# Optimization experiments

Measured on AMD Instinct MI355X. Metric: run time of the kernel, lower is better.

Reference implementation:

```python
import math
import jax, jax.numpy as jnp
import numpy as np

CNT_HEAD, D_IN, D_OUT, D_KEY, D_VALUE = 16, 1024, 1024, 64, 64
BATCH, SEQ = 4, 2048
IS_SCALED, IS_CAUSAL = True, True


def _xavier(key, shape, d1, d2):
    a = math.sqrt(6.0 / (d1 + d2))
    return jax.random.uniform(key, shape, jnp.float32, -a, a)


def setup_inputs() -> dict:
    key = jax.random.key(0)
    kx, kq, kk, kv, ko = jax.random.split(key, 5)
    x = jax.random.normal(kx, (BATCH, SEQ, D_IN), jnp.float32)
    mask = jnp.zeros((BATCH, SEQ), dtype=bool)  # padding mask, True = masked out
    W_q = _xavier(kq, (CNT_HEAD, D_IN, D_KEY), D_IN, CNT_HEAD * D_KEY)
    W_k = _xavier(kk, (CNT_HEAD, D_IN, D_KEY), D_IN, CNT_HEAD * D_KEY)
    W_v = _xavier(kv, (CNT_HEAD, D_IN, D_VALUE), D_IN, CNT_HEAD * D_VALUE)
    W_o = _xavier(ko, (CNT_HEAD, D_VALUE, D_OUT), CNT_HEAD * D_VALUE, D_OUT)
    return {"x": x, "mask": mask, "W_q": W_q, "W_k": W_k, "W_v": W_v, "W_o": W_o}


def reference(x, mask, W_q, W_k, W_v, W_o):
    seq_len = x.shape[-2]
    # per-head projections: (h, d_in, d) x (b, s, d_in) -> (b, h, s, d)
    Q = jnp.einsum('hjk,bsj->bhsk', W_q, x)
    K = jnp.einsum('hjk,bsj->bhsk', W_k, x)
    V = jnp.einsum('hjk,bsj->bhsk', W_v, x)
    # combined mask -> (b, 1, s, s), True = masked
    causal = jnp.triu(jnp.ones((seq_len, seq_len), dtype=bool), k=1)
    if IS_CAUSAL:
        m = mask[..., None, :] | causal  # (b, s, s)
    else:
        m = jnp.broadcast_to(mask[..., None, :], (mask.shape[0], seq_len, seq_len))
    m = m[..., None, :, :]  # (b, 1, s, s)
    scores = jnp.einsum('bhik,bhjk->bhij', Q, K)
    scores = jnp.where(m, -jnp.inf, scores)
    if IS_SCALED:
        scores = scores / math.sqrt(D_KEY)
    weights = jax.nn.softmax(scores, axis=-1)
    values = jnp.einsum('bhij,bhjd->bhid', weights, V)
    return jnp.einsum('hjk,bhlj->blk', W_o, values)
```

## Files before the change

### kernel.cpp

```cpp
#include <hip/hip_runtime.h>
#include <hip/hip_bf16.h>

typedef __attribute__((ext_vector_type(4))) float f32x4;
typedef __attribute__((ext_vector_type(8))) short s16x8;
typedef __attribute__((ext_vector_type(8))) unsigned short u16x8;
typedef __attribute__((ext_vector_type(4))) unsigned short u16x4;

#define BATCH 4
#define SEQ   2048
#define DIN   1024
#define NHEAD 16
#define HD3   3072
#define DOUT  1024

__device__ __forceinline__ unsigned short f2bf(float f) {
  __hip_bfloat16 h = __float2bfloat16(f);
  return __builtin_bit_cast(unsigned short, h);
}

__device__ __forceinline__ float fmax3(float a, float b, float c) {
  return fmaxf(fmaxf(a, b), c);
}

#if __has_builtin(__builtin_amdgcn_exp2f)
__device__ __forceinline__ float fast_exp2(float x) { return __builtin_amdgcn_exp2f(x); }
#else
__device__ __forceinline__ float fast_exp2(float x) { return exp2f(x); }
#endif

typedef const __attribute__((address_space(1))) unsigned int* gas_t;
typedef __attribute__((address_space(3))) unsigned int* las_t;
__device__ __forceinline__ void gload16(const void* g, void* l) {
  __builtin_amdgcn_global_load_lds((gas_t)g, (las_t)l, 16, 0, 0);
}

__global__ __launch_bounds__(256) void k_cvt_x(const float* __restrict__ x,
                                               unsigned short* __restrict__ xb, int n4) {
  int i = blockIdx.x * 256 + threadIdx.x;
  int stride = gridDim.x * 256;
  for (; i < n4; i += stride) {
    float4 v = reinterpret_cast<const float4*>(x)[i];
    ushort4 o;
    o.x = f2bf(v.x); o.y = f2bf(v.y); o.z = f2bf(v.z); o.w = f2bf(v.w);
    reinterpret_cast<ushort4*>(xb)[i] = o;
  }
}

__global__ __launch_bounds__(256) void k_cvt_w(const float* __restrict__ W,
                                               unsigned short* __restrict__ dst) {
  __shared__ float t[64][65];
  int h = blockIdx.x, j0 = blockIdx.y * 64;
  int c = threadIdx.x & 63, r0 = threadIdx.x >> 6;
#pragma unroll
  for (int r = r0; r < 64; r += 4)
    t[r][c] = W[h * 65536 + (j0 + r) * 64 + c];
  __syncthreads();
#pragma unroll
  for (int k = r0; k < 64; k += 4)
    dst[(size_t)(h * 64 + k) * 1024 + j0 + c] = f2bf(t[c][k]);
}

__global__ __launch_bounds__(256) void k_cvt_wo(const float* __restrict__ W,
                                                unsigned short* __restrict__ dst) {
  __shared__ float t[64][65];
  int h = blockIdx.x, n0 = blockIdx.y * 64;
  int c = threadIdx.x & 63, r0 = threadIdx.x >> 6;
#pragma unroll
  for (int d = r0; d < 64; d += 4)
    t[d][c] = W[h * 65536 + d * 1024 + n0 + c];
  __syncthreads();
#pragma unroll
  for (int n = r0; n < 64; n += 4)
    dst[(size_t)(n0 + n) * 1024 + h * 64 + c] = f2bf(t[c][n]);
}

__global__ __launch_bounds__(256) void k_transpose_v(const unsigned short* __restrict__ QKV,
                                                     unsigned short* __restrict__ Vt) {
  __shared__ unsigned short t[64 * 80];
  int tid = threadIdx.x;
  int s0 = blockIdx.x * 64;
  int h = blockIdx.y, b = blockIdx.z;
  const unsigned short* src = QKV + (size_t)b * SEQ * HD3 + 2048 + (size_t)h * 64;
#pragma unroll
  for (int c = 0; c < 2; ++c) {
    int slot = tid + c * 256;
    int s = slot >> 3, g = slot & 7;
    u16x8 v = *reinterpret_cast<const u16x8*>(src + (size_t)(s0 + s) * HD3 + g * 8);
    *reinterpret_cast<u16x8*>(&t[s * 80 + (g ^ (s >> 3)) * 8]) = v;
  }
  __syncthreads();
  unsigned short* dst = Vt + (size_t)(b * NHEAD + h) * 64 * SEQ + s0;
#pragma unroll
  for (int c = 0; c < 2; ++c) {
    int slot = tid + c * 256;
    int d = slot >> 3, c8 = slot & 7;
    u16x8 v;
#pragma unroll
    for (int j = 0; j < 8; ++j) {
      int s = ((c8 >> 2) << 5) + ((j >> 2) << 4) + ((c8 & 3) << 2) + (j & 3);
      v[j] = t[s * 80 + (((d >> 3) ^ (s >> 3)) * 8) + (d & 7)];
    }
    *reinterpret_cast<u16x8*>(dst + (size_t)d * SEQ + c8 * 8) = v;
  }
}

__device__ __forceinline__ void stout(float* p, float v) { *p = v; }
__device__ __forceinline__ void stout(unsigned short* p, float v) { *p = f2bf(v); }

template <typename OutT>
__global__ __launch_bounds__(256) void gemm_bt(const unsigned short* __restrict__ A,
                                               const unsigned short* __restrict__ Bt,
                                               OutT* __restrict__ C, int M, int N, int K) {
  __shared__ unsigned short As[3][128 * 32];
  __shared__ unsigned short Bs[3][128 * 32];
  int tid = threadIdx.x, w = tid >> 6, lane = tid & 63;
  int lr = lane & 15, lk = lane >> 4;
  int m0 = blockIdx.x * 128, n0 = blockIdx.y * 128;
  int wm = (w >> 1) * 64, wn = (w & 1) * 64;
  const f32x4 z = {0.f, 0.f, 0.f, 0.f};
  f32x4 acc[4][4];
#pragma unroll
  for (int m = 0; m < 4; ++m)
#pragma unroll
    for (int n = 0; n < 4; ++n) acc[m][n] = z;

  int r0 = w * 32 + (lane >> 2);
  int r1 = r0 + 16;
  int scol = (((lane & 3) ^ ((lane >> 2) & 3)) * 8);
  const unsigned short* pA0 = A + (size_t)(m0 + r0) * K + scol;
  const unsigned short* pA1 = A + (size_t)(m0 + r1) * K + scol;
  const unsigned short* pB0 = Bt + (size_t)(n0 + r0) * K + scol;
  const unsigned short* pB1 = Bt + (size_t)(n0 + r1) * K + scol;

#define GSTAGE(bi_, ko_)                                              \
  {                                                                   \
    gload16(pA0 + (ko_), (char*)As[bi_] + (w * 2 + 0) * 1024);        \
    gload16(pB0 + (ko_), (char*)Bs[bi_] + (w * 2 + 0) * 1024);        \
    gload16(pA1 + (ko_), (char*)As[bi_] + (w * 2 + 1) * 1024);        \
    gload16(pB1 + (ko_), (char*)Bs[bi_] + (w * 2 + 1) * 1024);        \
  }

  GSTAGE(0, 0)
  GSTAGE(1, 32)
  asm volatile("s_waitcnt vmcnt(4)" ::: "memory");
  __builtin_amdgcn_s_barrier();
  asm volatile("" ::: "memory");

  const int T = K >> 5;
  int bi = 0;
  int cka = lk ^ (lr & 3);
  for (int t = 0; t < T; ++t) {
    if (t + 2 < T) {
      int bs = bi + 2; if (bs >= 3) bs -= 3;
      GSTAGE(bs, (t + 2) * 32)
    }
    s16x8 af[4], bfr[4];
#pragma unroll
    for (int m = 0; m < 4; ++m)
      af[m] = *reinterpret_cast<const s16x8*>(&As[bi][(wm + m * 16 + lr) * 32 + cka * 8]);
#pragma unroll
    for (int n = 0; n < 4; ++n)
      bfr[n] = *reinterpret_cast<const s16x8*>(&Bs[bi][(wn + n * 16 + lr) * 32 + cka * 8]);
#pragma unroll
    for (int m = 0; m < 4; ++m)
#pragma unroll
      for (int n = 0; n < 4; ++n)
        acc[m][n] = __builtin_amdgcn_mfma_f32_16x16x32_bf16(af[m], bfr[n], acc[m][n], 0, 0, 0);
    asm volatile("s_waitcnt lgkmcnt(0)" ::: "memory");
    if (t + 2 < T)
      asm volatile("s_waitcnt vmcnt(4)" ::: "memory");
    else
      asm volatile("s_waitcnt vmcnt(0)" ::: "memory");
    __builtin_amdgcn_s_barrier();
    asm volatile("" ::: "memory");
    if (++bi >= 3) bi = 0;
  }
#undef GSTAGE

#pragma unroll
  for (int m = 0; m < 4; ++m)
#pragma unroll
    for (int n = 0; n < 4; ++n)
#pragma unroll
      for (int r = 0; r < 4; ++r) {
        int row = m0 + wm + m * 16 + lk * 4 + r;
        int col = n0 + wn + n * 16 + lr;
        stout(&C[(size_t)row * N + col], acc[m][n][r]);
      }
}

__global__ __launch_bounds__(256) void attn_kernel(const unsigned short* __restrict__ QKV,
                                                   const unsigned short* __restrict__ Vt,
                                                   unsigned short* __restrict__ Oa) {
  __shared__ unsigned short Ks[2][2][64 * 64];
  __shared__ unsigned short Vs[2][2][64 * 64];
  int tid = threadIdx.x, w = tid >> 6, lane = tid & 63;
  int lr = lane & 15, lk = lane >> 4;
  int bx = blockIdx.x;
  int bh = bx & 63;
  int qbi = 15 - (bx >> 6);
  int h = bh & 15, b = bh >> 4;
  int q0 = qbi * 128 + w * 32;
  const unsigned short* base = QKV + (size_t)b * SEQ * HD3;
  const unsigned short* vtb = Vt + (size_t)(b * NHEAD + h) * 64 * SEQ;
  const float cl = 0.1803368801111204f;
  const f32x4 z = {0.f, 0.f, 0.f, 0.f};

  s16x8 qf[2][2];
#pragma unroll
  for (int mf = 0; mf < 2; ++mf)
#pragma unroll
    for (int kfi = 0; kfi < 2; ++kfi)
      qf[mf][kfi] = *reinterpret_cast<const s16x8*>(
          base + (size_t)(q0 + mf * 16 + lr) * HD3 + h * 64 + kfi * 32 + lk * 8);

  f32x4 o[4][2], lacc[2];
#pragma unroll
  for (int nfd = 0; nfd < 4; ++nfd)
#pragma unroll
    for (int mf = 0; mf < 2; ++mf) o[nfd][mf] = z;
  lacc[0] = z; lacc[1] = z;
  float m_[2] = {-1e30f, -1e30f};
  s16x8 ones;
#pragma unroll
  for (int e = 0; e < 8; ++e) ones[e] = (short)0x3F80;

  const int nt = qbi + 1;

  int xr = (lr & 7) << 4;
  int off8[4][2];
#pragma unroll
  for (int nf = 0; nf < 4; ++nf)
#pragma unroll
    for (int kfi = 0; kfi < 2; ++kfi)
      off8[nf][kfi] = (nf * 16 + lr) * 128 + ((kfi * 64 + lk * 16) ^ xr);

  int srow0 = w * 16 + (lane >> 3);
  int cbs = ((lane & 7) * 16) ^ ((srow0 & 7) << 4);
  const char* pk0 = (const char*)(base + 1024 + h * 64 + (size_t)srow0 * HD3) + cbs;
  const char* pk1 = pk0 + (size_t)8 * HD3 * 2;
  const char* pv0 = (const char*)(vtb + (size_t)srow0 * SEQ) + cbs;
  const char* pv1 = pv0 + (size_t)8 * SEQ * 2;
  const size_t KSUB = (size_t)64 * HD3 * 2;
  const size_t KADV = (size_t)128 * HD3 * 2;
  const size_t VADV = 256;

#define STAGE(BS)                                                       \
  {                                                                     \
    gload16(pk0, (char*)&Ks[(BS)][0][0] + (w * 2 + 0) * 1024);          \
    gload16(pk0 + KSUB, (char*)&Ks[(BS)][1][0] + (w * 2 + 0) * 1024);   \
    gload16(pv0, (char*)&Vs[(BS)][0][0] + (w * 2 + 0) * 1024);          \
    gload16(pv0 + 128, (char*)&Vs[(BS)][1][0] + (w * 2 + 0) * 1024);    \
    gload16(pk1, (char*)&Ks[(BS)][0][0] + (w * 2 + 1) * 1024);          \
    gload16(pk1 + KSUB, (char*)&Ks[(BS)][1][0] + (w * 2 + 1) * 1024);   \
    gload16(pv1, (char*)&Vs[(BS)][0][0] + (w * 2 + 1) * 1024);          \
    gload16(pv1 + 128, (char*)&Vs[(BS)][1][0] + (w * 2 + 1) * 1024);    \
    pk0 += KADV; pk1 += KADV; pv0 += VADV; pv1 += VADV;                 \
  }

#define SUBTILE(BI, S, KB)                                                                \
  if ((KB) <= q0 + 31) {                                                                  \
    s16x8 kfr[4][2];                                                                      \
    _Pragma("unroll") for (int nf = 0; nf < 4; ++nf)                                      \
    _Pragma("unroll") for (int kfi = 0; kfi < 2; ++kfi)                                   \
      kfr[nf][kfi] = *reinterpret_cast<const s16x8*>(                                     \
          (const char*)&Ks[(BI)][(S)][0] + off8[nf][kfi]);                                \
    f32x4 st[4][2];                                                                       \
    _Pragma("unroll") for (int nf = 0; nf < 4; ++nf)                                      \
    _Pragma("unroll") for (int mf = 0; mf < 2; ++mf)                                      \
      st[nf][mf] = __builtin_amdgcn_mfma_f32_16x16x32_bf16(kfr[nf][0], qf[mf][0], z, 0, 0, 0); \
    _Pragma("unroll") for (int nf = 0; nf < 4; ++nf)                                      \
    _Pragma("unroll") for (int mf = 0; mf < 2; ++mf)                                      \
      st[nf][mf] = __builtin_amdgcn_mfma_f32_16x16x32_bf16(kfr[nf][1], qf[mf][1],         \
                                                           st[nf][mf], 0, 0, 0);          \
    if ((KB) + 63 > q0) {                                                                 \
      _Pragma("unroll") for (int nf = 0; nf < 4; ++nf)                                    \
      _Pragma("unroll") for (int mf = 0; mf < 2; ++mf)                                    \
      _Pragma("unroll") for (int r = 0; r < 4; ++r)                                       \
        if ((KB) + nf * 16 + lk * 4 + r > q0 + mf * 16 + lr) st[nf][mf][r] = -1e30f;      \
    }                                                                                     \
    s16x8 pf[2][2];                                                                       \
    _Pragma("unroll") for (int mf = 0; mf < 2; ++mf) {                                    \
      float t0 = fmax3(st[0][mf][0], st[0][mf][1], st[0][mf][2]);                         \
      float t1 = fmax3(st[0][mf][3], st[1][mf][0], st[1][mf][1]);                         \
      float t2 = fmax3(st[1][mf][2], st[1][mf][3], st[2][mf][0]);                         \
      float t3 = fmax3(st[2][mf][1], st[2][mf][2], st[2][mf][3]);                         \
      float t4 = fmax3(st[3][mf][0], st[3][mf][1], st[3][mf][2]);                         \
      float pm = fmaxf(fmax3(t0, t1, t2), fmax3(t3, t4, st[3][mf][3]));                   \
      pm = fmaxf(pm, __shfl_xor(pm, 16));                                                 \
      pm = fmaxf(pm, __shfl_xor(pm, 32));                                                 \
      pm *= cl;                                                                           \
      if (!__all(pm <= m_[mf] + 8.0f)) {                                                  \
        float mnew = fmaxf(m_[mf], pm);                                                   \
        float sc = fast_exp2(m_[mf] - mnew);                                              \
        m_[mf] = mnew;                                                                    \
        _Pragma("unroll") for (int nfd = 0; nfd < 4; ++nfd)                               \
        _Pragma("unroll") for (int r = 0; r < 4; ++r) o[nfd][mf][r] *= sc;                \
        _Pragma("unroll") for (int r = 0; r < 4; ++r) lacc[mf][r] *= sc;                  \
      }                                                                                   \
      float p[4][4];                                                                      \
      _Pragma("unroll") for (int nf = 0; nf < 4; ++nf)                                    \
      _Pragma("unroll") for (int r = 0; r < 4; ++r)                                       \
        p[nf][r] = fast_exp2(fmaf(st[nf][mf][r], cl, -m_[mf]));                           \
      union { s16x8 v; unsigned short e[8]; } pu0, pu1;                                   \
      _Pragma("unroll") for (int j2 = 0; j2 < 4; ++j2) {                                  \
        pu0.e[j2] = f2bf(p[0][j2]);                                                       \
        pu0.e[4 + j2] = f2bf(p[1][j2]);                                                   \
        pu1.e[j2] = f2bf(p[2][j2]);                                                       \
        pu1.e[4 + j2] = f2bf(p[3][j2]);                                                   \
      }                                                                                   \
      pf[mf][0] = pu0.v;                                                                  \
      pf[mf][1] = pu1.v;                                                                  \
    }                                                                                     \
    _Pragma("unroll") for (int mf = 0; mf < 2; ++mf)                                      \
    _Pragma("unroll") for (int ks = 0; ks < 2; ++ks)                                      \
      lacc[mf] = __builtin_amdgcn_mfma_f32_16x16x32_bf16(ones, pf[mf][ks],                \
                                                         lacc[mf], 0, 0, 0);              \
    _Pragma("unroll") for (int nfd = 0; nfd < 4; ++nfd)                                   \
    _Pragma("unroll") for (int ks = 0; ks < 2; ++ks) {                                    \
      s16x8 vf = *reinterpret_cast<const s16x8*>(                                         \
          (const char*)&Vs[(BI)][(S)][0] + off8[nfd][ks]);                                \
      _Pragma("unroll") for (int mf = 0; mf < 2; ++mf)                                    \
        o[nfd][mf] = __builtin_amdgcn_mfma_f32_16x16x32_bf16(vf, pf[mf][ks],              \
                                                             o[nfd][mf], 0, 0, 0);        \
    }                                                                                     \
  }

#define TILE(BI)                                                                          \
  {                                                                                       \
    if (kt + 1 < nt) STAGE((BI) ^ 1)                                                      \
    int kb = kt * 128;                                                                    \
    SUBTILE(BI, 0, kb)                                                                    \
    SUBTILE(BI, 1, kb + 64)                                                               \
    asm volatile("s_waitcnt lgkmcnt(0)" ::: "memory");                                    \
    asm volatile("s_waitcnt vmcnt(0)" ::: "memory");                                      \
    __builtin_amdgcn_s_barrier();                                                         \
    asm volatile("" ::: "memory");                                                        \
    ++kt;                                                                                 \
  }

  STAGE(0)
  asm volatile("s_waitcnt vmcnt(0)" ::: "memory");
  __builtin_amdgcn_s_barrier();
  asm volatile("" ::: "memory");

  int kt = 0;
  for (;;) {
    TILE(0)
    if (kt == nt) break;
    TILE(1)
    if (kt == nt) break;
  }
#undef TILE
#undef SUBTILE
#undef STAGE

#pragma unroll
  for (int mf = 0; mf < 2; ++mf) {
    float inv = 1.0f / lacc[mf][0];
    size_t rowoff = (size_t)(b * SEQ + q0 + mf * 16 + lr) * 1024 + h * 64;
#pragma unroll
    for (int nfd = 0; nfd < 4; ++nfd) {
      u16x4 ov;
#pragma unroll
      for (int r = 0; r < 4; ++r) ov[r] = f2bf(o[nfd][mf][r] * inv);
      *reinterpret_cast<u16x4*>(Oa + rowoff + nfd * 16 + lk * 4) = ov;
    }
  }
}

extern "C" void kernel_launch(void* const* d_in, const int* in_sizes, int n_in,
                              void* d_out, int out_size, void* d_ws, size_t ws_size,
                              hipStream_t stream) {
  const float* x  = (const float*)d_in[0];
  const float* Wq = (const float*)d_in[2];
  const float* Wk = (const float*)d_in[3];
  const float* Wv = (const float*)d_in[4];
  const float* Wo = (const float*)d_in[5];
  float* out = (float*)d_out;

  char* ws = (char*)d_ws;
  unsigned short* xb   = (unsigned short*)(ws);
  unsigned short* Wqkv = (unsigned short*)(ws + 16777216);
  unsigned short* Wot  = (unsigned short*)(ws + 23068672);
  unsigned short* QKV  = (unsigned short*)(ws + 25165824);
  unsigned short* Oa   = (unsigned short*)(ws + 75497472);
  unsigned short* Vtp  = xb;

  k_cvt_x<<<2048, 256, 0, stream>>>(x, xb, (BATCH * SEQ * DIN) / 4);
  dim3 wg(16, 16);
  k_cvt_w<<<wg, 256, 0, stream>>>(Wq, Wqkv);
  k_cvt_w<<<wg, 256, 0, stream>>>(Wk, Wqkv + 1024 * 1024);
  k_cvt_w<<<wg, 256, 0, stream>>>(Wv, Wqkv + 2 * 1024 * 1024);
  k_cvt_wo<<<wg, 256, 0, stream>>>(Wo, Wot);

  gemm_bt<unsigned short><<<dim3(64, 24), 256, 0, stream>>>(xb, Wqkv, QKV, 8192, 3072, 1024);
  k_transpose_v<<<dim3(32, NHEAD, BATCH), 256, 0, stream>>>(QKV, Vtp);
  attn_kernel<<<dim3(1024), 256, 0, stream>>>(QKV, Vtp, Oa);
  gemm_bt<float><<<dim3(64, 8), 256, 0, stream>>>(Oa, Wot, out, 8192, 1024, 1024);
}
```

Before: 199.8 us.

## Fuse V transpose into QKV GEMM epilogue and merge weight conversions

The QKV projection GEMM now writes the V columns directly in transposed per-head layout to a separate buffer, and stores only Q and K with row stride 2048. This removes the standalone V transpose kernel and its extra read and write of V. The four weight-conversion launches are also merged into one kernel indexed by blockIdx.z, cutting launch overhead. In exchange, the V epilogue does strided 8-byte stores across sequence rows, which may coalesce less well than the old row-major stores.

```diff
diff --git a/kernel.cpp b/kernel.cpp
--- a/kernel.cpp
+++ b/kernel.cpp
@@ -10,7 +10,7 @@
 #define SEQ   2048
 #define DIN   1024
 #define NHEAD 16
-#define HD3   3072
+#define QKW   2048
 #define DOUT  1024
 
 __device__ __forceinline__ unsigned short f2bf(float f) {
@@ -46,61 +46,34 @@
   }
 }
 
-__global__ __launch_bounds__(256) void k_cvt_w(const float* __restrict__ W,
-                                               unsigned short* __restrict__ dst) {
+__global__ __launch_bounds__(256) void k_cvt_wall(const float* __restrict__ Wq,
+                                                  const float* __restrict__ Wk,
+                                                  const float* __restrict__ Wv,
+                                                  const float* __restrict__ Wo,
+                                                  unsigned short* __restrict__ Wqkv,
+                                                  unsigned short* __restrict__ Wot) {
   __shared__ float t[64][65];
-  int h = blockIdx.x, j0 = blockIdx.y * 64;
+  int zi = blockIdx.z;
   int c = threadIdx.x & 63, r0 = threadIdx.x >> 6;
-#pragma unroll
-  for (int r = r0; r < 64; r += 4)
-    t[r][c] = W[h * 65536 + (j0 + r) * 64 + c];
-  __syncthreads();
-#pragma unroll
-  for (int k = r0; k < 64; k += 4)
-    dst[(size_t)(h * 64 + k) * 1024 + j0 + c] = f2bf(t[c][k]);
-}
-
-__global__ __launch_bounds__(256) void k_cvt_wo(const float* __restrict__ W,
-                                                unsigned short* __restrict__ dst) {
-  __shared__ float t[64][65];
-  int h = blockIdx.x, n0 = blockIdx.y * 64;
-  int c = threadIdx.x & 63, r0 = threadIdx.x >> 6;
-#pragma unroll
-  for (int d = r0; d < 64; d += 4)
-    t[d][c] = W[h * 65536 + d * 1024 + n0 + c];
-  __syncthreads();
-#pragma unroll
-  for (int n = r0; n < 64; n += 4)
-    dst[(size_t)(n0 + n) * 1024 + h * 64 + c] = f2bf(t[c][n]);
-}
-
-__global__ __launch_bounds__(256) void k_transpose_v(const unsigned short* __restrict__ QKV,
-                                                     unsigned short* __restrict__ Vt) {
-  __shared__ unsigned short t[64 * 80];
-  int tid = threadIdx.x;
-  int s0 = blockIdx.x * 64;
-  int h = blockIdx.y, b = blockIdx.z;
-  const unsigned short* src = QKV + (size_t)b * SEQ * HD3 + 2048 + (size_t)h * 64;
-#pragma unroll
-  for (int c = 0; c < 2; ++c) {
-    int slot = tid + c * 256;
-    int s = slot >> 3, g = slot & 7;
-    u16x8 v = *reinterpret_cast<const u16x8*>(src + (size_t)(s0 + s) * HD3 + g * 8);
-    *reinterpret_cast<u16x8*>(&t[s * 80 + (g ^ (s >> 3)) * 8]) = v;
-  }
-  __syncthreads();
-  unsigned short* dst = Vt + (size_t)(b * NHEAD + h) * 64 * SEQ + s0;
-#pragma unroll
-  for (int c = 0; c < 2; ++c) {
-    int slot = tid + c * 256;
-    int d = slot >> 3, c8 = slot & 7;
-    u16x8 v;
-#pragma unroll
-    for (int j = 0; j < 8; ++j) {
-      int s = ((c8 >> 2) << 5) + ((j >> 2) << 4) + ((c8 & 3) << 2) + (j & 3);
-      v[j] = t[s * 80 + (((d >> 3) ^ (s >> 3)) * 8) + (d & 7)];
-    }
-    *reinterpret_cast<u16x8*>(dst + (size_t)d * SEQ + c8 * 8) = v;
+  int hb = blockIdx.x, g0 = blockIdx.y * 64;
+  if (zi < 3) {
+    const float* W = (zi == 0) ? Wq : ((zi == 1) ? Wk : Wv);
+    unsigned short* dst = Wqkv + (size_t)zi * 1024 * 1024;
+#pragma unroll
+    for (int r = r0; r < 64; r += 4)
+      t[r][c] = W[hb * 65536 + (g0 + r) * 64 + c];
+    __syncthreads();
+#pragma unroll
+    for (int k = r0; k < 64; k += 4)
+      dst[(size_t)(hb * 64 + k) * 1024 + g0 + c] = f2bf(t[c][k]);
+  } else {
+#pragma unroll
+    for (int d = r0; d < 64; d += 4)
+      t[d][c] = Wo[hb * 65536 + d * 1024 + g0 + c];
+    __syncthreads();
+#pragma unroll
+    for (int n = r0; n < 64; n += 4)
+      Wot[(size_t)(g0 + n) * 1024 + hb * 64 + c] = f2bf(t[c][n]);
   }
 }
 
@@ -110,7 +83,8 @@
 template <typename OutT>
 __global__ __launch_bounds__(256) void gemm_bt(const unsigned short* __restrict__ A,
                                                const unsigned short* __restrict__ Bt,
-                                               OutT* __restrict__ C, int M, int N, int K) {
+                                               OutT* __restrict__ C, int M, int N, int K,
+                                               int NC, unsigned short* __restrict__ VtOut) {
   __shared__ unsigned short As[3][128 * 32];
   __shared__ unsigned short Bs[3][128 * 32];
   int tid = threadIdx.x, w = tid >> 6, lane = tid & 63;
@@ -177,19 +151,38 @@
   }
 #undef GSTAGE
 
-#pragma unroll
-  for (int m = 0; m < 4; ++m)
-#pragma unroll
-    for (int n = 0; n < 4; ++n)
-#pragma unroll
-      for (int r = 0; r < 4; ++r) {
-        int row = m0 + wm + m * 16 + lk * 4 + r;
-        int col = n0 + wn + n * 16 + lr;
-        stout(&C[(size_t)row * N + col], acc[m][n][r]);
+  if (VtOut != nullptr && n0 >= 2048) {
+    int hh = (n0 + wn - 2048) >> 6;
+    int bb = (m0 + wm) >> 11;
+    int sb = (m0 + wm) & 2047;
+#pragma unroll
+    for (int m = 0; m < 4; ++m) {
+      int p64 = ((m >> 1) & 1) * 32 + lk * 8 + (m & 1) * 4;
+#pragma unroll
+      for (int n = 0; n < 4; ++n) {
+        int d = n * 16 + lr;
+        u16x4 ov;
+#pragma unroll
+        for (int r = 0; r < 4; ++r) ov[r] = f2bf(acc[m][n][r]);
+        *reinterpret_cast<u16x4*>(
+            &VtOut[((size_t)(bb * NHEAD + hh) * 64 + d) * SEQ + sb + p64]) = ov;
       }
-}
-
-__global__ __launch_bounds__(256) void attn_kernel(const unsigned short* __restrict__ QKV,
+    }
+  } else {
+#pragma unroll
+    for (int m = 0; m < 4; ++m)
+#pragma unroll
+      for (int n = 0; n < 4; ++n)
+#pragma unroll
+        for (int r = 0; r < 4; ++r) {
+          int row = m0 + wm + m * 16 + lk * 4 + r;
+          int col = n0 + wn + n * 16 + lr;
+          stout(&C[(size_t)row * NC + col], acc[m][n][r]);
+        }
+  }
+}
+
+__global__ __launch_bounds__(256) void attn_kernel(const unsigned short* __restrict__ QK,
                                                    const unsigned short* __restrict__ Vt,
                                                    unsigned short* __restrict__ Oa) {
   __shared__ unsigned short Ks[2][2][64 * 64];
@@ -201,7 +194,7 @@
   int qbi = 15 - (bx >> 6);
   int h = bh & 15, b = bh >> 4;
   int q0 = qbi * 128 + w * 32;
-  const unsigned short* base = QKV + (size_t)b * SEQ * HD3;
+  const unsigned short* base = QK + (size_t)b * SEQ * QKW;
   const unsigned short* vtb = Vt + (size_t)(b * NHEAD + h) * 64 * SEQ;
   const float cl = 0.1803368801111204f;
   const f32x4 z = {0.f, 0.f, 0.f, 0.f};
@@ -212,7 +205,7 @@
 #pragma unroll
     for (int kfi = 0; kfi < 2; ++kfi)
       qf[mf][kfi] = *reinterpret_cast<const s16x8*>(
-          base + (size_t)(q0 + mf * 16 + lr) * HD3 + h * 64 + kfi * 32 + lk * 8);
+          base + (size_t)(q0 + mf * 16 + lr) * QKW + h * 64 + kfi * 32 + lk * 8);
 
   f32x4 o[4][2], lacc[2];
 #pragma unroll
@@ -237,12 +230,12 @@
 
   int srow0 = w * 16 + (lane >> 3);
   int cbs = ((lane & 7) * 16) ^ ((srow0 & 7) << 4);
-  const char* pk0 = (const char*)(base + 1024 + h * 64 + (size_t)srow0 * HD3) + cbs;
-  const char* pk1 = pk0 + (size_t)8 * HD3 * 2;
+  const char* pk0 = (const char*)(base + 1024 + h * 64 + (size_t)srow0 * QKW) + cbs;
+  const char* pk1 = pk0 + (size_t)8 * QKW * 2;
   const char* pv0 = (const char*)(vtb + (size_t)srow0 * SEQ) + cbs;
   const char* pv1 = pv0 + (size_t)8 * SEQ * 2;
-  const size_t KSUB = (size_t)64 * HD3 * 2;
-  const size_t KADV = (size_t)128 * HD3 * 2;
+  const size_t KSUB = (size_t)64 * QKW * 2;
+  const size_t KADV = (size_t)128 * QKW * 2;
   const size_t VADV = 256;
 
 #define STAGE(BS)                                                       \
@@ -383,19 +376,16 @@
   unsigned short* xb   = (unsigned short*)(ws);
   unsigned short* Wqkv = (unsigned short*)(ws + 16777216);
   unsigned short* Wot  = (unsigned short*)(ws + 23068672);
-  unsigned short* QKV  = (unsigned short*)(ws + 25165824);
+  unsigned short* QK   = (unsigned short*)(ws + 25165824);
+  unsigned short* Vt   = (unsigned short*)(ws + 58720256);
   unsigned short* Oa   = (unsigned short*)(ws + 75497472);
-  unsigned short* Vtp  = xb;
 
   k_cvt_x<<<2048, 256, 0, stream>>>(x, xb, (BATCH * SEQ * DIN) / 4);
-  dim3 wg(16, 16);
-  k_cvt_w<<<wg, 256, 0, stream>>>(Wq, Wqkv);
-  k_cvt_w<<<wg, 256, 0, stream>>>(Wk, Wqkv + 1024 * 1024);
-  k_cvt_w<<<wg, 256, 0, stream>>>(Wv, Wqkv + 2 * 1024 * 1024);
-  k_cvt_wo<<<wg, 256, 0, stream>>>(Wo, Wot);
-
-  gemm_bt<unsigned short><<<dim3(64, 24), 256, 0, stream>>>(xb, Wqkv, QKV, 8192, 3072, 1024);
-  k_transpose_v<<<dim3(32, NHEAD, BATCH), 256, 0, stream>>>(QKV, Vtp);
-  attn_kernel<<<dim3(1024), 256, 0, stream>>>(QKV, Vtp, Oa);
-  gemm_bt<float><<<dim3(64, 8), 256, 0, stream>>>(Oa, Wot, out, 8192, 1024, 1024);
-}
+  k_cvt_wall<<<dim3(16, 16, 4), 256, 0, stream>>>(Wq, Wk, Wv, Wo, Wqkv, Wot);
+
+  gemm_bt<unsigned short><<<dim3(64, 24), 256, 0, stream>>>(xb, Wqkv, QK, 8192, 3072, 1024,
+                                                            2048, Vt);
+  attn_kernel<<<dim3(1024), 256, 0, stream>>>(QK, Vt, Oa);
+  gemm_bt<float><<<dim3(64, 8), 256, 0, stream>>>(Oa, Wot, out, 8192, 1024, 1024, 1024,
+                                                  nullptr);
+}
```

After: 175.5 us. 12.2% less time.
